# Kernel optimization log

Hardware: AMD Instinct MI355X
Metric: run time of the kernel (lower is better)

## Reference

```python
import jax, jax.numpy as jnp
import numpy as np

SR = 44100
D = SR * 30          # duration_samples = 1_323_000
N = 1024             # number of note events
L = 32768            # max note length in samples
W = 1024             # hann window length (module's window_length)
H = 8                # harmonics in the synth
K = 128              # FIR taps in the effect chain
LAT = 2              # time_latent_size


def setup_inputs() -> dict:
    key = jax.random.key(0)
    ks = jax.random.split(key, 10)
    freq_rad = jax.random.uniform(ks[0], (N,), jnp.float32, 0.01, 0.3)
    velocity = jax.random.uniform(ks[1], (N,), jnp.float32, 1.0, 127.0)
    starts = jax.random.randint(ks[2], (N,), 0, D - L, dtype=jnp.int32)
    lengths = jax.random.randint(ks[3], (N,), 2048, L + 1, dtype=jnp.int32)
    # time_embedder: Linear(1,32) -> ReLU -> Linear(32,LAT)
    w1 = jax.random.normal(ks[4], (1, 32), jnp.float32)
    b1 = jnp.zeros((32,), jnp.float32)
    w2 = jax.random.normal(ks[5], (32, LAT), jnp.float32) / jnp.sqrt(32.0)
    b2 = jnp.zeros((LAT,), jnp.float32)
    # synth amplitude MLP: [freq, vel, latent] (2+LAT) -> 64 -> H
    ws1 = jax.random.normal(ks[6], (2 + LAT, 64), jnp.float32)
    bs1 = jnp.zeros((64,), jnp.float32)
    ws2 = jax.random.normal(ks[7], (64, H), jnp.float32) / 8.0
    bs2 = jnp.zeros((H,), jnp.float32)
    # effect chain: causal FIR (OIW layout) + tanh
    fir = jax.random.normal(ks[8], (1, 1, K), jnp.float32) / K
    return dict(freq_rad=freq_rad, velocity=velocity,
                w1=w1, b1=b1, w2=w2, b2=b2,
                ws1=ws1, bs1=bs1, ws2=ws2, bs2=bs2, fir=fir,
                starts=starts, lengths=lengths, duration_samples=D)


def reference(freq_rad, velocity, w1, b1, w2, b2, ws1, bs1, ws2, bs2, fir,
              starts, lengths, duration_samples):
    Dn = int(duration_samples)
    t = jnp.arange(L, dtype=jnp.float32)            # [L]
    ti = jnp.arange(L, dtype=jnp.int32)             # [L]
    ends = starts + lengths
    # output_length = min(end, duration) - start, clipped to [0, L]
    out_len = jnp.clip(jnp.minimum(ends, Dn) - starts, 0, L)  # [N]
    # time latent: MLP on normalized start time
    nt = (starts.astype(jnp.float32) / Dn)[:, None]           # [N,1]
    lat = jax.nn.relu(nt @ w1 + b1) @ w2 + b2                  # [N,LAT]
    vel = (velocity / 127.0)[:, None]                          # [N,1]
    # harmonic amplitudes from tiny MLP (the 'synth')
    feat = jnp.concatenate([freq_rad[:, None], vel, lat], axis=-1)  # [N,2+LAT]
    amps = jax.nn.softplus(jax.nn.relu(feat @ ws1 + bs1) @ ws2 + bs2)  # [N,H]
    # additive synthesis; fixed small loop over harmonics, vectorized over [N,L]
    phase = freq_rad[:, None] * t[None, :]                     # [N,L]
    seg = jnp.zeros((N, L), jnp.float32)
    for hh in range(1, H + 1):
        seg = seg + amps[:, hh - 1:hh] * jnp.sin(hh * phase)
    seg = seg * vel
    # hann window (torch periodic) on the LAST W samples of each variable-length segment
    n = jnp.arange(W, dtype=jnp.float32)
    hann = 0.5 * (1.0 - jnp.cos(2.0 * jnp.pi * n / W))         # [W]
    wpos = ti[None, :] - (out_len[:, None] - W)                # [N,L]
    in_win = (wpos >= 0) & (wpos < W)
    factor = jnp.where(in_win, hann[jnp.clip(wpos, 0, W - 1)], 1.0)
    mask = (ti[None, :] < out_len[:, None]).astype(jnp.float32)  # zero past segment end
    seg = seg * factor * mask
    # effect chain: causal 128-tap FIR then tanh (masked so padding stays silent)
    y = jax.lax.conv_general_dilated(seg[:, None, :], fir,
                                     window_strides=(1,), padding=[(K - 1, 0)])
    seg = jnp.tanh(y[:, 0, :]) * mask                          # [N,L]
    # overlap-add: scatter each note into the output buffer
    idx = starts[:, None] + ti[None, :]                        # [N,L]
    valid = (ti[None, :] < out_len[:, None]) & (idx < Dn)
    contrib = jnp.where(valid, seg, 0.0)
    out = jnp.zeros((Dn,), jnp.float32).at[jnp.clip(idx, 0, Dn - 1).reshape(-1)].add(
        contrib.reshape(-1))
    return out
```

## Files before the change

### kernel.cpp

```cpp
#include <hip/hip_runtime.h>
#include <math.h>

#define LMAX  32768
#define WWIN  1024
#define KFIR  128
#define WOUT  1024
#define TO    1024
#define CPAD  1232
#define SYNTH 1152
#define ZPS   1148
#define NMAX  1024
#define SLOT  128

typedef _Float16 v8h __attribute__((ext_vector_type(8)));
typedef _Float16 v4h __attribute__((ext_vector_type(4)));
typedef float    v4f __attribute__((ext_vector_type(4)));

__device__ __forceinline__ float fast_tanh(float x) {
    float e = __builtin_amdgcn_exp2f(x * 2.8853900817779268f);
    return fmaf(-2.0f, __builtin_amdgcn_rcpf(e + 1.0f), 1.0f);
}

__global__ __launch_bounds__(256) void setup_notes_k(
    const float* __restrict__ freq_g, const float* __restrict__ velo_g,
    const float* __restrict__ w1,  const float* __restrict__ b1,
    const float* __restrict__ w2,  const float* __restrict__ b2,
    const float* __restrict__ ws1, const float* __restrict__ bs1,
    const float* __restrict__ ws2, const float* __restrict__ bs2,
    const int* __restrict__ starts, const int* __restrict__ lengths,
    float* __restrict__ npar, int* __restrict__ counts,
    unsigned short* __restrict__ lists,
    int Dn, int N, int n_tiles)
{
    __shared__ float s_w1[32], s_b1[32], s_w2[64], s_b2[2];
    __shared__ float s_ws1[256], s_bs1[64], s_ws2[512], s_bs2[8];
    const int tid = threadIdx.x;
    if (tid < 32) { s_w1[tid] = w1[tid]; s_b1[tid] = b1[tid]; }
    if (tid < 64) { s_w2[tid] = w2[tid]; s_bs1[tid] = bs1[tid]; }
    if (tid < 2)  s_b2[tid] = b2[tid];
    if (tid < 8)  s_bs2[tid] = bs2[tid];
    s_ws1[tid] = ws1[tid];
    s_ws2[tid] = ws2[tid];  s_ws2[tid + 256] = ws2[tid + 256];
    __syncthreads();

    const int j = blockIdx.x * 256 + tid;
    if (j >= N) return;

    int st  = starts[j];
    int len = lengths[j];
    int ol  = min(st + len, Dn) - st;
    ol = max(0, min(ol, LMAX));
    float v = velo_g[j] * (1.0f / 127.0f);
    float f = freq_g[j];
    float nt = (float)st / (float)Dn;
    float lat0 = s_b2[0], lat1 = s_b2[1];
    #pragma unroll
    for (int jj = 0; jj < 32; ++jj) {
        float h = fmaxf(fmaf(nt, s_w1[jj], s_b1[jj]), 0.0f);
        lat0 = fmaf(h, s_w2[jj * 2 + 0], lat0);
        lat1 = fmaf(h, s_w2[jj * 2 + 1], lat1);
    }
    float acc[8];
    #pragma unroll
    for (int h = 0; h < 8; ++h) acc[h] = s_bs2[h];
    #pragma unroll
    for (int jj = 0; jj < 64; ++jj) {
        float a = s_bs1[jj];
        a = fmaf(f,    s_ws1[0 * 64 + jj], a);
        a = fmaf(v,    s_ws1[1 * 64 + jj], a);
        a = fmaf(lat0, s_ws1[2 * 64 + jj], a);
        a = fmaf(lat1, s_ws1[3 * 64 + jj], a);
        a = fmaxf(a, 0.0f);
        #pragma unroll
        for (int h = 0; h < 8; ++h)
            acc[h] = fmaf(a, s_ws2[jj * 8 + h], acc[h]);
    }
    float* p = npar + (size_t)j * 12;
    p[0] = __int_as_float(st);
    p[1] = __int_as_float(ol);
    p[2] = f;
    p[3] = 0.0f;
    #pragma unroll
    for (int h = 0; h < 8; ++h) {
        float a = acc[h];
        float sp = fmaxf(a, 0.0f) + log1pf(expf(-fabsf(a)));
        p[4 + h] = sp * v;
    }

    if (ol > 0) {
        int t0 = st >> 10;
        int t1 = min((st + ol - 1) >> 10, n_tiles - 1);
        for (int t = t0; t <= t1; ++t) {
            int pos = atomicAdd(&counts[t], 1);
            if (pos < SLOT) lists[(size_t)t * SLOT + pos] = (unsigned short)j;
        }
    }
}

__global__ __launch_bounds__(1024) void sort_tiles_k(
    const int* __restrict__ counts, int* __restrict__ order, int n_tiles)
{
    __shared__ int hist[SLOT + 2];
    __shared__ int bstart[SLOT + 2];
    const int tid = threadIdx.x;
    if (tid < SLOT + 2) hist[tid] = 0;
    __syncthreads();
    for (int t = tid; t < n_tiles; t += 1024) {
        int k = min(counts[t], SLOT + 1);
        atomicAdd(&hist[k], 1);
    }
    __syncthreads();
    if (tid == 0) {
        int run = 0;
        for (int k = SLOT + 1; k >= 0; --k) { bstart[k] = run; run += hist[k]; }
    }
    __syncthreads();
    for (int t = tid; t < n_tiles; t += 1024) {
        int k = min(counts[t], SLOT + 1);
        int p = atomicAdd(&bstart[k], 1);
        order[p] = t;
    }
}

__global__ __launch_bounds__(256, 3) void synth_fused_k(
    const float* __restrict__ fir,
    const float* __restrict__ npar,
    const int* __restrict__ counts,
    const unsigned short* __restrict__ lists,
    const int* __restrict__ order,
    float* __restrict__ out, int Dn)
{
    __shared__ __align__(16) _Float16 segc[4][4][CPAD];
    __shared__ float fir_s[KFIR];
    __shared__ int   stl[SLOT], oll[SLOT];
    __shared__ float fl[SLOT];
    __shared__ __align__(16) float ampsl[SLOT][8];

    const int tid  = threadIdx.x;
    const int wid  = tid >> 6;
    const int lane = tid & 63;
    const int m    = lane & 15;
    const int quad = lane >> 4;
    const int grp  = wid;
    const int tile = order[blockIdx.x];
    const int o0   = tile * TO;
    const int ow   = o0;

    const int K = min(counts[tile], SLOT);

    if (tid < KFIR) fir_s[tid] = fir[tid];
    if (tid < K) {
        const int nid = (int)lists[(size_t)tile * SLOT + tid];
        const float4* pp = (const float4*)(npar + (size_t)nid * 12);
        float4 a = pp[0], b = pp[1], c = pp[2];
        stl[tid] = __float_as_int(a.x);
        oll[tid] = __float_as_int(a.y);
        fl[tid]  = a.z;
        *(float4*)&ampsl[tid][0] = b;
        *(float4*)&ampsl[tid][4] = c;
    }
    __syncthreads();

    v8h afrag[12];
    #pragma unroll
    for (int t = 0; t < 12; ++t) {
        v8h af;
        #pragma unroll
        for (int j = 0; j < 8; ++j) {
            int idx = 32 * t + 8 * quad + j - 16 * m;
            float fv = (idx >= 0 && idx < KFIR) ? fir_s[idx] : 0.0f;
            af[j] = (_Float16)fv;
        }
        afrag[t] = af;
    }
    for (int z = lane; z < 4 * (CPAD - ZPS); z += 64) {
        int S = z / (CPAD - ZPS), off = z % (CPAD - ZPS);
        segc[wid][S][ZPS + off] = (_Float16)0.0f;
    }

    const _Float16* __restrict__ bbase = &segc[wid][m & 3][(m & ~3) + 8 * quad];

    float accv[16];
    #pragma unroll
    for (int r = 0; r < 16; ++r) accv[r] = 0.0f;

    const double inv2pi = 0.15915494309189535;

    int stN = 0, olN = 0; float fN = 0.f;
    float4 amN0 = {}, amN1 = {};
    if (grp < K) {
        stN = stl[grp]; olN = oll[grp]; fN = fl[grp];
        amN0 = *(const float4*)&ampsl[grp][0];
        amN1 = *(const float4*)&ampsl[grp][4];
    }

    for (int kk = grp; kk < K; kk += 4) {
        const int st = stN, ol = olN;
        const float f = fN;
        const float4 am0 = amN0, am1 = amN1;
        if (kk + 4 < K) {
            stN = stl[kk + 4]; olN = oll[kk + 4]; fN = fl[kk + 4];
            amN0 = *(const float4*)&ampsl[kk + 4][0];
            amN1 = *(const float4*)&ampsl[kk + 4][4];
        }

        const int base = ow - st;
        if (base >= ol || base + WOUT <= 0) continue;

        const float A0 = am0.x, A1 = am0.y, A2 = am0.z, A3 = am0.w;
        const float A4 = am1.x, A5 = am1.y, A6 = am1.z, A7 = am1.w;
        const double fd = (double)f;

        const int tseed = base - 127 + lane;
        double rev0 = fd * (double)tseed * inv2pi;
        float r0 = (float)(rev0 - floor(rev0));
        float s = __builtin_amdgcn_sinf(r0);
        float cc = __builtin_amdgcn_cosf(r0);
        double d64 = fd * 64.0 * inv2pi;
        float r64 = (float)(d64 - floor(d64));
        const float sd = __builtin_amdgcn_sinf(r64);
        const float cd = __builtin_amdgcn_cosf(r64);
        const int wbase = ol - WWIN;

        const bool interior = (base >= 127) && (base + WOUT + 1 <= wbase);

        if (interior) {
            #pragma unroll
            for (int i = 0; i < SYNTH / 64; ++i) {
                float tc = cc + cc;
                float sA = s;
                float sum = A0 * sA;
                float sB = tc * sA;              sum = fmaf(A1, sB, sum);
                float sC = fmaf(tc, sB, -sA);    sum = fmaf(A2, sC, sum);
                float sD = fmaf(tc, sC, -sB);    sum = fmaf(A3, sD, sum);
                float sE = fmaf(tc, sD, -sC);    sum = fmaf(A4, sE, sum);
                float sF = fmaf(tc, sE, -sD);    sum = fmaf(A5, sF, sum);
                float sG = fmaf(tc, sF, -sE);    sum = fmaf(A6, sG, sum);
                float sH = fmaf(tc, sG, -sF);    sum = fmaf(A7, sH, sum);
                _Float16 h = (_Float16)sum;
                const int x = lane + 64 * i;
                if (i == 0) {
                    #pragma unroll
                    for (int S = 0; S < 4; ++S)
                        if (x >= S) segc[wid][S][x - S] = h;
                } else {
                    #pragma unroll
                    for (int S = 0; S < 4; ++S)
                        segc[wid][S][x - S] = h;
                }
                float ns = fmaf(s, cd, cc * sd);
                float nc = fmaf(cc, cd, -(s * sd));
                s = ns; cc = nc;
            }
        } else {
            #pragma unroll
            for (int i = 0; i < SYNTH / 64; ++i) {
                int t = tseed + 64 * i;
                float val = 0.0f;
                if (t >= 0 && t < ol) {
                    float tc = cc + cc;
                    float sA = s;
                    float sum = A0 * sA;
                    float sB = tc * sA;              sum = fmaf(A1, sB, sum);
                    float sC = fmaf(tc, sB, -sA);    sum = fmaf(A2, sC, sum);
                    float sD = fmaf(tc, sC, -sB);    sum = fmaf(A3, sD, sum);
                    float sE = fmaf(tc, sD, -sC);    sum = fmaf(A4, sE, sum);
                    float sF = fmaf(tc, sE, -sD);    sum = fmaf(A5, sF, sum);
                    float sG = fmaf(tc, sF, -sE);    sum = fmaf(A6, sG, sum);
                    float sH = fmaf(tc, sG, -sF);    sum = fmaf(A7, sH, sum);
                    int wpos = t - wbase;
                    float factor = 1.0f;
                    if (wpos >= 0)
                        factor = 0.5f - 0.5f * __builtin_amdgcn_cosf((float)wpos * (1.0f / WWIN));
                    val = sum * factor;
                }
                _Float16 h = (_Float16)val;
                const int x = lane + 64 * i;
                if (i == 0) {
                    #pragma unroll
                    for (int S = 0; S < 4; ++S)
                        if (x >= S) segc[wid][S][x - S] = h;
                } else {
                    #pragma unroll
                    for (int S = 0; S < 4; ++S)
                        segc[wid][S][x - S] = h;
                }
                float ns = fmaf(s, cd, cc * sd);
                float nc = fmaf(cc, cd, -(s * sd));
                s = ns; cc = nc;
            }
        }

        #pragma unroll
        for (int p = 0; p < 2; ++p) {
            const int co = 512 * p;
            v4f CA0 = {0.f, 0.f, 0.f, 0.f};
            v4f CA1 = {0.f, 0.f, 0.f, 0.f};
            v4f CB0 = {0.f, 0.f, 0.f, 0.f};
            v4f CB1 = {0.f, 0.f, 0.f, 0.f};
            #pragma unroll
            for (int t = 0; t < 6; ++t) {
                v4h lo = *(const v4h*)(bbase + co + 32 * t);
                v4h hi = *(const v4h*)(bbase + co + 32 * t + 4);
                v8h bf = __builtin_shufflevector(lo, hi, 0, 1, 2, 3, 4, 5, 6, 7);
                CA0 = __builtin_amdgcn_mfma_f32_16x16x32_f16(afrag[t], bf, CA0, 0, 0, 0);
                v4h lo2 = *(const v4h*)(bbase + co + 256 + 32 * t);
                v4h hi2 = *(const v4h*)(bbase + co + 256 + 32 * t + 4);
                v8h bf2 = __builtin_shufflevector(lo2, hi2, 0, 1, 2, 3, 4, 5, 6, 7);
                CB0 = __builtin_amdgcn_mfma_f32_16x16x32_f16(afrag[t], bf2, CB0, 0, 0, 0);
            }
            #pragma unroll
            for (int t = 6; t < 12; ++t) {
                v4h lo = *(const v4h*)(bbase + co + 32 * t);
                v4h hi = *(const v4h*)(bbase + co + 32 * t + 4);
                v8h bf = __builtin_shufflevector(lo, hi, 0, 1, 2, 3, 4, 5, 6, 7);
                CA1 = __builtin_amdgcn_mfma_f32_16x16x32_f16(afrag[t], bf, CA1, 0, 0, 0);
                v4h lo2 = *(const v4h*)(bbase + co + 256 + 32 * t);
                v4h hi2 = *(const v4h*)(bbase + co + 256 + 32 * t + 4);
                v8h bf2 = __builtin_shufflevector(lo2, hi2, 0, 1, 2, 3, 4, 5, 6, 7);
                CB1 = __builtin_amdgcn_mfma_f32_16x16x32_f16(afrag[t], bf2, CB1, 0, 0, 0);
            }

            const int tb = base + co + 64 * quad + m;
            float y;
            y = CA0[0] + CA1[0]; if (tb +   0 >= 0 && tb +   0 < ol) accv[p*8+0] += fast_tanh(y);
            y = CA0[1] + CA1[1]; if (tb +  16 >= 0 && tb +  16 < ol) accv[p*8+1] += fast_tanh(y);
            y = CA0[2] + CA1[2]; if (tb +  32 >= 0 && tb +  32 < ol) accv[p*8+2] += fast_tanh(y);
            y = CA0[3] + CA1[3]; if (tb +  48 >= 0 && tb +  48 < ol) accv[p*8+3] += fast_tanh(y);
            y = CB0[0] + CB1[0]; if (tb + 256 >= 0 && tb + 256 < ol) accv[p*8+4] += fast_tanh(y);
            y = CB0[1] + CB1[1]; if (tb + 272 >= 0 && tb + 272 < ol) accv[p*8+5] += fast_tanh(y);
            y = CB0[2] + CB1[2]; if (tb + 288 >= 0 && tb + 288 < ol) accv[p*8+6] += fast_tanh(y);
            y = CB0[3] + CB1[3]; if (tb + 304 >= 0 && tb + 304 < ol) accv[p*8+7] += fast_tanh(y);
        }
    }

    __syncthreads();
    float* red = (float*)&segc[0][0][0];
    const int slot0 = 64 * quad + m;
    if (grp != 0) {
        float* rg = red + (grp - 1) * 1024;
        #pragma unroll
        for (int p = 0; p < 2; ++p) {
            #pragma unroll
            for (int r = 0; r < 8; ++r) {
                const int idx = slot0 + 512 * p + (r >> 2) * 256 + (r & 3) * 16;
                rg[idx] = accv[p * 8 + r];
            }
        }
    }
    __syncthreads();
    if (grp == 0) {
        #pragma unroll
        for (int p = 0; p < 2; ++p) {
            #pragma unroll
            for (int r = 0; r < 8; ++r) {
                const int idx = slot0 + 512 * p + (r >> 2) * 256 + (r & 3) * 16;
                float v = accv[p * 8 + r] + red[idx] + red[1024 + idx] + red[2048 + idx];
                const int ob = o0 + idx;
                if (ob < Dn) out[ob] = v;
            }
        }
    }
}

extern "C" void kernel_launch(void* const* d_in, const int* in_sizes, int n_in,
                              void* d_out, int out_size, void* d_ws, size_t ws_size,
                              hipStream_t stream) {
    const float* freq    = (const float*)d_in[0];
    const float* velo    = (const float*)d_in[1];
    const float* w1      = (const float*)d_in[2];
    const float* b1      = (const float*)d_in[3];
    const float* w2      = (const float*)d_in[4];
    const float* b2      = (const float*)d_in[5];
    const float* ws1     = (const float*)d_in[6];
    const float* bs1     = (const float*)d_in[7];
    const float* ws2     = (const float*)d_in[8];
    const float* bs2     = (const float*)d_in[9];
    const float* fir     = (const float*)d_in[10];
    const int*   starts  = (const int*)d_in[11];
    const int*   lengths = (const int*)d_in[12];

    const int N  = in_sizes[0];
    const int Dn = out_size;
    float* out = (float*)d_out;

    const int n_tiles = (Dn + TO - 1) / TO;

    char* ws = (char*)d_ws;
    float* npar = (float*)ws;
    size_t off1 = ((size_t)N * 12 * sizeof(float) + 255) & ~(size_t)255;
    int* counts = (int*)(ws + off1);
    size_t off2 = off1 + (((size_t)n_tiles * sizeof(int) + 255) & ~(size_t)255);
    unsigned short* lists = (unsigned short*)(ws + off2);
    size_t off3 = off2 + (((size_t)n_tiles * SLOT * sizeof(unsigned short) + 255) & ~(size_t)255);
    int* order = (int*)(ws + off3);

    hipMemsetAsync(counts, 0, (size_t)n_tiles * sizeof(int), stream);
    setup_notes_k<<<(N + 255) / 256, 256, 0, stream>>>(
        freq, velo, w1, b1, w2, b2, ws1, bs1, ws2, bs2,
        starts, lengths, npar, counts, lists, Dn, N, n_tiles);
    sort_tiles_k<<<1, 1024, 0, stream>>>(counts, order, n_tiles);
    synth_fused_k<<<n_tiles, 256, 0, stream>>>(
        fir, npar, counts, lists, order, out, Dn);
}
```

Before: 148.8 us.

## Fuse setup and tile sort into one block; pack synth recurrence into float2

The memset, per-note setup kernel and tile-sort kernel are merged into a single 1024-thread block that counts per-tile notes in shared memory, which removes two launches and the global atomics. The synth loop now processes two 64-sample strides per iteration as float2 vectors so the compiler can emit packed FMA instructions, and the phase step grows to 128 samples. The trade-off is that all note setup runs serially on one block, and the longer recurrence step may add small phase error.

```diff
diff --git a/kernel.cpp b/kernel.cpp
--- a/kernel.cpp
+++ b/kernel.cpp
@@ -9,19 +9,20 @@
 #define CPAD  1232
 #define SYNTH 1152
 #define ZPS   1148
-#define NMAX  1024
 #define SLOT  128
+#define MAXT  2048
 
 typedef _Float16 v8h __attribute__((ext_vector_type(8)));
 typedef _Float16 v4h __attribute__((ext_vector_type(4)));
 typedef float    v4f __attribute__((ext_vector_type(4)));
+typedef float    v2f __attribute__((ext_vector_type(2)));
 
 __device__ __forceinline__ float fast_tanh(float x) {
     float e = __builtin_amdgcn_exp2f(x * 2.8853900817779268f);
     return fmaf(-2.0f, __builtin_amdgcn_rcpf(e + 1.0f), 1.0f);
 }
 
-__global__ __launch_bounds__(256) void setup_notes_k(
+__global__ __launch_bounds__(1024) void setup_all_k(
     const float* __restrict__ freq_g, const float* __restrict__ velo_g,
     const float* __restrict__ w1,  const float* __restrict__ b1,
     const float* __restrict__ w2,  const float* __restrict__ b2,
@@ -29,85 +30,82 @@
     const float* __restrict__ ws2, const float* __restrict__ bs2,
     const int* __restrict__ starts, const int* __restrict__ lengths,
     float* __restrict__ npar, int* __restrict__ counts,
-    unsigned short* __restrict__ lists,
+    unsigned short* __restrict__ lists, int* __restrict__ order,
     int Dn, int N, int n_tiles)
 {
     __shared__ float s_w1[32], s_b1[32], s_w2[64], s_b2[2];
     __shared__ float s_ws1[256], s_bs1[64], s_ws2[512], s_bs2[8];
+    __shared__ int   cnt_s[MAXT];
+    __shared__ int   hist[SLOT + 2];
+    __shared__ int   bstart[SLOT + 2];
+
     const int tid = threadIdx.x;
-    if (tid < 32) { s_w1[tid] = w1[tid]; s_b1[tid] = b1[tid]; }
-    if (tid < 64) { s_w2[tid] = w2[tid]; s_bs1[tid] = bs1[tid]; }
-    if (tid < 2)  s_b2[tid] = b2[tid];
-    if (tid < 8)  s_bs2[tid] = bs2[tid];
-    s_ws1[tid] = ws1[tid];
-    s_ws2[tid] = ws2[tid];  s_ws2[tid + 256] = ws2[tid + 256];
-    __syncthreads();
-
-    const int j = blockIdx.x * 256 + tid;
-    if (j >= N) return;
-
-    int st  = starts[j];
-    int len = lengths[j];
-    int ol  = min(st + len, Dn) - st;
-    ol = max(0, min(ol, LMAX));
-    float v = velo_g[j] * (1.0f / 127.0f);
-    float f = freq_g[j];
-    float nt = (float)st / (float)Dn;
-    float lat0 = s_b2[0], lat1 = s_b2[1];
-    #pragma unroll
-    for (int jj = 0; jj < 32; ++jj) {
-        float h = fmaxf(fmaf(nt, s_w1[jj], s_b1[jj]), 0.0f);
-        lat0 = fmaf(h, s_w2[jj * 2 + 0], lat0);
-        lat1 = fmaf(h, s_w2[jj * 2 + 1], lat1);
-    }
-    float acc[8];
-    #pragma unroll
-    for (int h = 0; h < 8; ++h) acc[h] = s_bs2[h];
-    #pragma unroll
-    for (int jj = 0; jj < 64; ++jj) {
-        float a = s_bs1[jj];
-        a = fmaf(f,    s_ws1[0 * 64 + jj], a);
-        a = fmaf(v,    s_ws1[1 * 64 + jj], a);
-        a = fmaf(lat0, s_ws1[2 * 64 + jj], a);
-        a = fmaf(lat1, s_ws1[3 * 64 + jj], a);
-        a = fmaxf(a, 0.0f);
-        #pragma unroll
-        for (int h = 0; h < 8; ++h)
-            acc[h] = fmaf(a, s_ws2[jj * 8 + h], acc[h]);
-    }
-    float* p = npar + (size_t)j * 12;
-    p[0] = __int_as_float(st);
-    p[1] = __int_as_float(ol);
-    p[2] = f;
-    p[3] = 0.0f;
-    #pragma unroll
-    for (int h = 0; h < 8; ++h) {
-        float a = acc[h];
-        float sp = fmaxf(a, 0.0f) + log1pf(expf(-fabsf(a)));
-        p[4 + h] = sp * v;
-    }
-
-    if (ol > 0) {
-        int t0 = st >> 10;
-        int t1 = min((st + ol - 1) >> 10, n_tiles - 1);
-        for (int t = t0; t <= t1; ++t) {
-            int pos = atomicAdd(&counts[t], 1);
-            if (pos < SLOT) lists[(size_t)t * SLOT + pos] = (unsigned short)j;
-        }
-    }
-}
-
-__global__ __launch_bounds__(1024) void sort_tiles_k(
-    const int* __restrict__ counts, int* __restrict__ order, int n_tiles)
-{
-    __shared__ int hist[SLOT + 2];
-    __shared__ int bstart[SLOT + 2];
-    const int tid = threadIdx.x;
+    if (tid < 32)  { s_w1[tid] = w1[tid]; s_b1[tid] = b1[tid]; }
+    if (tid < 64)  { s_w2[tid] = w2[tid]; s_bs1[tid] = bs1[tid]; }
+    if (tid < 2)   s_b2[tid] = b2[tid];
+    if (tid < 8)   s_bs2[tid] = bs2[tid];
+    if (tid < 256) s_ws1[tid] = ws1[tid];
+    if (tid < 512) s_ws2[tid] = ws2[tid];
+    for (int t = tid; t < n_tiles; t += 1024) cnt_s[t] = 0;
     if (tid < SLOT + 2) hist[tid] = 0;
     __syncthreads();
+
+    for (int j = tid; j < N; j += 1024) {
+        int st  = starts[j];
+        int len = lengths[j];
+        int ol  = min(st + len, Dn) - st;
+        ol = max(0, min(ol, LMAX));
+        float v = velo_g[j] * (1.0f / 127.0f);
+        float f = freq_g[j];
+        float nt = (float)st / (float)Dn;
+        float lat0 = s_b2[0], lat1 = s_b2[1];
+        #pragma unroll
+        for (int jj = 0; jj < 32; ++jj) {
+            float h = fmaxf(fmaf(nt, s_w1[jj], s_b1[jj]), 0.0f);
+            lat0 = fmaf(h, s_w2[jj * 2 + 0], lat0);
+            lat1 = fmaf(h, s_w2[jj * 2 + 1], lat1);
+        }
+        float acc[8];
+        #pragma unroll
+        for (int h = 0; h < 8; ++h) acc[h] = s_bs2[h];
+        #pragma unroll
+        for (int jj = 0; jj < 64; ++jj) {
+            float a = s_bs1[jj];
+            a = fmaf(f,    s_ws1[0 * 64 + jj], a);
+            a = fmaf(v,    s_ws1[1 * 64 + jj], a);
+            a = fmaf(lat0, s_ws1[2 * 64 + jj], a);
+            a = fmaf(lat1, s_ws1[3 * 64 + jj], a);
+            a = fmaxf(a, 0.0f);
+            #pragma unroll
+            for (int h = 0; h < 8; ++h)
+                acc[h] = fmaf(a, s_ws2[jj * 8 + h], acc[h]);
+        }
+        float* p = npar + (size_t)j * 12;
+        p[0] = __int_as_float(st);
+        p[1] = __int_as_float(ol);
+        p[2] = f;
+        p[3] = 0.0f;
+        #pragma unroll
+        for (int h = 0; h < 8; ++h) {
+            float a = acc[h];
+            float sp = fmaxf(a, 0.0f) + log1pf(expf(-fabsf(a)));
+            p[4 + h] = sp * v;
+        }
+        if (ol > 0) {
+            int t0 = st >> 10;
+            int t1 = min((st + ol - 1) >> 10, n_tiles - 1);
+            for (int t = t0; t <= t1; ++t) {
+                int pos = atomicAdd(&cnt_s[t], 1);
+                if (pos < SLOT) lists[(size_t)t * SLOT + pos] = (unsigned short)j;
+            }
+        }
+    }
+    __syncthreads();
+
     for (int t = tid; t < n_tiles; t += 1024) {
-        int k = min(counts[t], SLOT + 1);
-        atomicAdd(&hist[k], 1);
+        int c = cnt_s[t];
+        counts[t] = c;
+        atomicAdd(&hist[min(c, SLOT + 1)], 1);
     }
     __syncthreads();
     if (tid == 0) {
@@ -116,7 +114,7 @@
     }
     __syncthreads();
     for (int t = tid; t < n_tiles; t += 1024) {
-        int k = min(counts[t], SLOT + 1);
+        int k = min(cnt_s[t], SLOT + 1);
         int p = atomicAdd(&bstart[k], 1);
         order[p] = t;
     }
@@ -207,86 +205,110 @@
         const int base = ow - st;
         if (base >= ol || base + WOUT <= 0) continue;
 
-        const float A0 = am0.x, A1 = am0.y, A2 = am0.z, A3 = am0.w;
-        const float A4 = am1.x, A5 = am1.y, A6 = am1.z, A7 = am1.w;
+        const v2f A0v = {am0.x, am0.x}, A1v = {am0.y, am0.y};
+        const v2f A2v = {am0.z, am0.z}, A3v = {am0.w, am0.w};
+        const v2f A4v = {am1.x, am1.x}, A5v = {am1.y, am1.y};
+        const v2f A6v = {am1.z, am1.z}, A7v = {am1.w, am1.w};
         const double fd = (double)f;
 
         const int tseed = base - 127 + lane;
         double rev0 = fd * (double)tseed * inv2pi;
-        float r0 = (float)(rev0 - floor(rev0));
-        float s = __builtin_amdgcn_sinf(r0);
-        float cc = __builtin_amdgcn_cosf(r0);
-        double d64 = fd * 64.0 * inv2pi;
-        float r64 = (float)(d64 - floor(d64));
-        const float sd = __builtin_amdgcn_sinf(r64);
-        const float cd = __builtin_amdgcn_cosf(r64);
+        double d64  = fd * 64.0 * inv2pi;
+        double rev1 = rev0 + d64;
+        double d128 = d64 + d64;
+        float r0   = (float)(rev0 - floor(rev0));
+        float r1   = (float)(rev1 - floor(rev1));
+        float r128 = (float)(d128 - floor(d128));
+        v2f s  = { __builtin_amdgcn_sinf(r0), __builtin_amdgcn_sinf(r1) };
+        v2f cc = { __builtin_amdgcn_cosf(r0), __builtin_amdgcn_cosf(r1) };
+        const float sd128 = __builtin_amdgcn_sinf(r128);
+        const float cd128 = __builtin_amdgcn_cosf(r128);
+        const v2f sdv = {sd128, sd128}, cdv = {cd128, cd128};
         const int wbase = ol - WWIN;
 
         const bool interior = (base >= 127) && (base + WOUT + 1 <= wbase);
 
         if (interior) {
             #pragma unroll
-            for (int i = 0; i < SYNTH / 64; ++i) {
-                float tc = cc + cc;
-                float sA = s;
-                float sum = A0 * sA;
-                float sB = tc * sA;              sum = fmaf(A1, sB, sum);
-                float sC = fmaf(tc, sB, -sA);    sum = fmaf(A2, sC, sum);
-                float sD = fmaf(tc, sC, -sB);    sum = fmaf(A3, sD, sum);
-                float sE = fmaf(tc, sD, -sC);    sum = fmaf(A4, sE, sum);
-                float sF = fmaf(tc, sE, -sD);    sum = fmaf(A5, sF, sum);
-                float sG = fmaf(tc, sF, -sE);    sum = fmaf(A6, sG, sum);
-                float sH = fmaf(tc, sG, -sF);    sum = fmaf(A7, sH, sum);
-                _Float16 h = (_Float16)sum;
-                const int x = lane + 64 * i;
-                if (i == 0) {
+            for (int j = 0; j < SYNTH / 128; ++j) {
+                v2f tc = cc + cc;
+                v2f sA = s;
+                v2f sum = sA * A0v;
+                v2f sB = tc * sA;                                 sum = __builtin_elementwise_fma(A1v, sB, sum);
+                v2f sC = __builtin_elementwise_fma(tc, sB, -sA);  sum = __builtin_elementwise_fma(A2v, sC, sum);
+                v2f sD = __builtin_elementwise_fma(tc, sC, -sB);  sum = __builtin_elementwise_fma(A3v, sD, sum);
+                v2f sE = __builtin_elementwise_fma(tc, sD, -sC);  sum = __builtin_elementwise_fma(A4v, sE, sum);
+                v2f sF = __builtin_elementwise_fma(tc, sE, -sD);  sum = __builtin_elementwise_fma(A5v, sF, sum);
+                v2f sG = __builtin_elementwise_fma(tc, sF, -sE);  sum = __builtin_elementwise_fma(A6v, sG, sum);
+                v2f sH = __builtin_elementwise_fma(tc, sG, -sF);  sum = __builtin_elementwise_fma(A7v, sH, sum);
+                _Float16 h0 = (_Float16)sum.x;
+                _Float16 h1 = (_Float16)sum.y;
+                const int x0 = lane + 128 * j;
+                const int x1 = x0 + 64;
+                if (j == 0) {
                     #pragma unroll
                     for (int S = 0; S < 4; ++S)
-                        if (x >= S) segc[wid][S][x - S] = h;
+                        if (x0 >= S) segc[wid][S][x0 - S] = h0;
                 } else {
                     #pragma unroll
                     for (int S = 0; S < 4; ++S)
-                        segc[wid][S][x - S] = h;
+                        segc[wid][S][x0 - S] = h0;
                 }
-                float ns = fmaf(s, cd, cc * sd);
-                float nc = fmaf(cc, cd, -(s * sd));
+                #pragma unroll
+                for (int S = 0; S < 4; ++S)
+                    segc[wid][S][x1 - S] = h1;
+                v2f ns = __builtin_elementwise_fma(s, cdv, cc * sdv);
+                v2f nc = __builtin_elementwise_fma(cc, cdv, -(s * sdv));
                 s = ns; cc = nc;
             }
         } else {
             #pragma unroll
-            for (int i = 0; i < SYNTH / 64; ++i) {
-                int t = tseed + 64 * i;
-                float val = 0.0f;
-                if (t >= 0 && t < ol) {
-                    float tc = cc + cc;
-                    float sA = s;
-                    float sum = A0 * sA;
-                    float sB = tc * sA;              sum = fmaf(A1, sB, sum);
-                    float sC = fmaf(tc, sB, -sA);    sum = fmaf(A2, sC, sum);
-                    float sD = fmaf(tc, sC, -sB);    sum = fmaf(A3, sD, sum);
-                    float sE = fmaf(tc, sD, -sC);    sum = fmaf(A4, sE, sum);
-                    float sF = fmaf(tc, sE, -sD);    sum = fmaf(A5, sF, sum);
-                    float sG = fmaf(tc, sF, -sE);    sum = fmaf(A6, sG, sum);
-                    float sH = fmaf(tc, sG, -sF);    sum = fmaf(A7, sH, sum);
-                    int wpos = t - wbase;
+            for (int j = 0; j < SYNTH / 128; ++j) {
+                const int t0 = tseed + 128 * j;
+                const int t1 = t0 + 64;
+                v2f tc = cc + cc;
+                v2f sA = s;
+                v2f sum = sA * A0v;
+                v2f sB = tc * sA;                                 sum = __builtin_elementwise_fma(A1v, sB, sum);
+                v2f sC = __builtin_elementwise_fma(tc, sB, -sA);  sum = __builtin_elementwise_fma(A2v, sC, sum);
+                v2f sD = __builtin_elementwise_fma(tc, sC, -sB);  sum = __builtin_elementwise_fma(A3v, sD, sum);
+                v2f sE = __builtin_elementwise_fma(tc, sD, -sC);  sum = __builtin_elementwise_fma(A4v, sE, sum);
+                v2f sF = __builtin_elementwise_fma(tc, sE, -sD);  sum = __builtin_elementwise_fma(A5v, sF, sum);
+                v2f sG = __builtin_elementwise_fma(tc, sF, -sE);  sum = __builtin_elementwise_fma(A6v, sG, sum);
+                v2f sH = __builtin_elementwise_fma(tc, sG, -sF);  sum = __builtin_elementwise_fma(A7v, sH, sum);
+                float v0 = 0.0f, v1 = 0.0f;
+                if (t0 >= 0 && t0 < ol) {
                     float factor = 1.0f;
+                    int wpos = t0 - wbase;
                     if (wpos >= 0)
                         factor = 0.5f - 0.5f * __builtin_amdgcn_cosf((float)wpos * (1.0f / WWIN));
-                    val = sum * factor;
+                    v0 = sum.x * factor;
                 }
-                _Float16 h = (_Float16)val;
-                const int x = lane + 64 * i;
-                if (i == 0) {
+                if (t1 >= 0 && t1 < ol) {
+                    float factor = 1.0f;
+                    int wpos = t1 - wbase;
+                    if (wpos >= 0)
+                        factor = 0.5f - 0.5f * __builtin_amdgcn_cosf((float)wpos * (1.0f / WWIN));
+                    v1 = sum.y * factor;
+                }
+                _Float16 h0 = (_Float16)v0;
+                _Float16 h1 = (_Float16)v1;
+                const int x0 = lane + 128 * j;
+                const int x1 = x0 + 64;
+                if (j == 0) {
                     #pragma unroll
                     for (int S = 0; S < 4; ++S)
-                        if (x >= S) segc[wid][S][x - S] = h;
+                        if (x0 >= S) segc[wid][S][x0 - S] = h0;
                 } else {
                     #pragma unroll
                     for (int S = 0; S < 4; ++S)
-                        segc[wid][S][x - S] = h;
+                        segc[wid][S][x0 - S] = h0;
                 }
-                float ns = fmaf(s, cd, cc * sd);
-                float nc = fmaf(cc, cd, -(s * sd));
+                #pragma unroll
+                for (int S = 0; S < 4; ++S)
+                    segc[wid][S][x1 - S] = h1;
+                v2f ns = __builtin_elementwise_fma(s, cdv, cc * sdv);
+                v2f nc = __builtin_elementwise_fma(cc, cdv, -(s * sdv));
                 s = ns; cc = nc;
             }
         }
@@ -395,11 +417,9 @@
     size_t off3 = off2 + (((size_t)n_tiles * SLOT * sizeof(unsigned short) + 255) & ~(size_t)255);
     int* order = (int*)(ws + off3);
 
-    hipMemsetAsync(counts, 0, (size_t)n_tiles * sizeof(int), stream);
-    setup_notes_k<<<(N + 255) / 256, 256, 0, stream>>>(
+    setup_all_k<<<1, 1024, 0, stream>>>(
         freq, velo, w1, b1, w2, b2, ws1, bs1, ws2, bs2,
-        starts, lengths, npar, counts, lists, Dn, N, n_tiles);
-    sort_tiles_k<<<1, 1024, 0, stream>>>(counts, order, n_tiles);
+        starts, lengths, npar, counts, lists, order, Dn, N, n_tiles);
     synth_fused_k<<<n_tiles, 256, 0, stream>>>(
         fir, npar, counts, lists, order, out, Dn);
 }
```

Measured after the change: 204.9 us. 1.38x slower.
